# Kernel optimization log

Measured on AMD Instinct MI355X. Metric: run time of the kernel, lower is better.

Reference implementation:

```python
import jax, jax.numpy as jnp
import numpy as np
import math

DIM = 1024
N_HEADS = 16
N_KV_HEADS = 8
HEAD_DIM = 64
HIDDEN = 4096
WINDOW = 512
NORM_EPS = 1e-5
QK_EPS = 1e-6


def get_alibi_slopes(n_heads):
    def _power_of_2(n):
        start = 2 ** (-2 ** (-(math.log2(n) - 3)))
        return [start * start ** i for i in range(n)]
    if math.log2(n_heads).is_integer():
        return _power_of_2(n_heads)
    closest = 2 ** math.floor(math.log2(n_heads))
    slopes = _power_of_2(closest)
    extra = _power_of_2(2 * closest)
    slopes.extend(extra[0::2][:n_heads - closest])
    return slopes


def layer_norm(x, w, eps):
    m = x.mean(-1, keepdims=True)
    v = ((x - m) ** 2).mean(-1, keepdims=True)
    return (x - m) * jax.lax.rsqrt(v + eps) * w


def setup_inputs() -> dict:
    key = jax.random.key(0)
    ks = jax.random.split(key, 16)
    s = 0.02
    return {
        "x": jax.random.normal(ks[0], (2, 2048, DIM), dtype=jnp.float32),
        "wq": jax.random.normal(ks[1], (N_HEADS * HEAD_DIM, DIM), dtype=jnp.float32) * s,
        "wk": jax.random.normal(ks[2], (N_KV_HEADS * HEAD_DIM, DIM), dtype=jnp.float32) * s,
        "wv": jax.random.normal(ks[3], (N_KV_HEADS * HEAD_DIM, DIM), dtype=jnp.float32) * s,
        "wo": jax.random.normal(ks[4], (DIM, N_HEADS * HEAD_DIM), dtype=jnp.float32) * s,
        "q_norm_w": jnp.ones((N_HEADS * HEAD_DIM,), dtype=jnp.float32),
        "k_norm_w": jnp.ones((N_KV_HEADS * HEAD_DIM,), dtype=jnp.float32),
        "attn_norm_w": jnp.ones((DIM,), dtype=jnp.float32),
        "ffn_norm_w": jnp.ones((DIM,), dtype=jnp.float32),
        "w1": jax.random.normal(ks[5], (HIDDEN, DIM), dtype=jnp.float32) * s,
        "w2": jax.random.normal(ks[6], (DIM, HIDDEN), dtype=jnp.float32) * s,
        "w3": jax.random.normal(ks[7], (HIDDEN, DIM), dtype=jnp.float32) * s,
        "attn_scale": jnp.full((DIM,), 1e-5, dtype=jnp.float32),
        "ffn_scale": jnp.full((DIM,), 1e-5, dtype=jnp.float32),
    }


def reference(x, wq, wk, wv, wo, q_norm_w, k_norm_w, attn_norm_w, ffn_norm_w,
              w1, w2, w3, attn_scale, ffn_scale):
    bsz, seqlen, _ = x.shape
    n_rep = N_HEADS // N_KV_HEADS

    h = layer_norm(x, attn_norm_w, NORM_EPS)
    q = layer_norm(h @ wq.T, q_norm_w, QK_EPS).reshape(bsz, seqlen, N_HEADS, HEAD_DIM).transpose(0, 2, 1, 3)
    k = layer_norm(h @ wk.T, k_norm_w, QK_EPS).reshape(bsz, seqlen, N_KV_HEADS, HEAD_DIM).transpose(0, 2, 1, 3)
    v = (h @ wv.T).reshape(bsz, seqlen, N_KV_HEADS, HEAD_DIM).transpose(0, 2, 1, 3)
    k = jnp.repeat(k, n_rep, axis=1)  # [b, H, s, hd]
    v = jnp.repeat(v, n_rep, axis=1)

    pos = jnp.arange(seqlen)
    dist = pos[None, :] - pos[:, None]  # dist[i, j] = j - i (as in the torch code)
    base = jnp.where((dist >= 0) & (dist <= WINDOW), 0.0, -jnp.inf)  # [s, s]
    slopes = jnp.asarray(get_alibi_slopes(N_HEADS), dtype=jnp.float32)
    alibi = -jnp.abs(slopes[:, None, None] * dist.astype(jnp.float32))  # [H, s, s]
    full_mask = base[None, :, :] + alibi  # [H, s, s]

    scores = jnp.einsum('bhqd,bhkd->bhqk', q, k) / math.sqrt(HEAD_DIM) + full_mask[None]
    attn = jax.nn.softmax(scores, axis=-1)
    out = jnp.einsum('bhqk,bhkd->bhqd', attn, v)
    out = out.transpose(0, 2, 1, 3).reshape(bsz, seqlen, N_HEADS * HEAD_DIM)
    x = x + (out @ wo.T) * attn_scale

    h2 = layer_norm(x, ffn_norm_w, NORM_EPS)
    ffn = (jax.nn.silu(h2 @ w1.T) * (h2 @ w3.T)) @ w2.T
    return x + ffn * ffn_scale
```

## Files before the change

kernel.cpp:

```cpp
#include <hip/hip_runtime.h>


typedef __bf16 bf16;
typedef __attribute__((ext_vector_type(8))) __bf16 bf16x8;
typedef __attribute__((ext_vector_type(4))) float f32x4;
typedef __attribute__((ext_vector_type(4))) short s16x4;

#define MFMA16(a, b, c) __builtin_amdgcn_mfma_f32_16x16x32_bf16(a, b, c, 0, 0, 0)

__device__ __forceinline__ void gload_lds16(const bf16* g, bf16* l) {
    __builtin_amdgcn_global_load_lds(
        (const __attribute__((address_space(1))) unsigned int*)g,
        (__attribute__((address_space(3))) unsigned int*)l, 16, 0, 0);
}

__global__ void sniff_kernel(const unsigned short* __restrict__ x, int* __restrict__ flag) {
    __shared__ int s;
    if (threadIdx.x == 0) s = 0;
    __syncthreads();
    int bad = 0;
#pragma unroll
    for (int i = 0; i < 16; ++i) {
        const unsigned short u = x[threadIdx.x * 16 + i];
        const int e = (u >> 7) & 0xFF;
        if (e >= 135) bad = 1;
    }
    if (bad) atomicOr(&s, 1);
    __syncthreads();
    if (threadIdx.x == 0) flag[0] = s;
}

__global__ void convert_all_kernel(const void* __restrict__ wq, const void* __restrict__ wk,
                                   const void* __restrict__ wv, const void* __restrict__ wo,
                                   const void* __restrict__ w1, const void* __restrict__ w3,
                                   const void* __restrict__ w2, bf16* __restrict__ dst,
                                   const int* __restrict__ flag) {
    const long e = ((long)blockIdx.x * 256 + threadIdx.x) * 4;
    const void* src; long off;
    if      (e < 1048576)  { src = wq; off = 0; }
    else if (e < 1572864)  { src = wk; off = 1048576; }
    else if (e < 2097152)  { src = wv; off = 1572864; }
    else if (e < 3145728)  { src = wo; off = 2097152; }
    else if (e < 7340032)  { src = w1; off = 3145728; }
    else if (e < 11534336) { src = w3; off = 7340032; }
    else                   { src = w2; off = 11534336; }
    if (flag[0] != 0) {
        const f32x4 v = *(const f32x4*)((const float*)src + (e - off));
        bf16 tmp[4];
#pragma unroll
        for (int j = 0; j < 4; ++j) tmp[j] = (bf16)v[j];
        *(s16x4*)(dst + e) = *(s16x4*)tmp;
    } else {
        *(s16x4*)(dst + e) = *(const s16x4*)((const short*)src + (e - off));
    }
}

__global__ void ln_kernel(const void* __restrict__ in, const void* __restrict__ w,
                          bf16* __restrict__ out, int W, float eps,
                          const int* __restrict__ flag, int in_flv, int w_flv) {
    const int row = blockIdx.x, t = threadIdx.x;
    const int nch = W >> 3;
    const bool act = t < nch;
    const bool f32 = flag[0] != 0;
    float v[8];
    float s = 0.f, s2 = 0.f;
    if (act) {
        if (in_flv && f32) {
            const float* rp = (const float*)in + (size_t)row * W + t * 8;
            const f32x4 a = *(const f32x4*)rp, b = *(const f32x4*)(rp + 4);
#pragma unroll
            for (int j = 0; j < 4; ++j) { v[j] = a[j]; v[4 + j] = b[j]; }
        } else {
            const bf16x8 xv = *(const bf16x8*)((const bf16*)in + (size_t)row * W + t * 8);
#pragma unroll
            for (int j = 0; j < 8; ++j) v[j] = (float)xv[j];
        }
#pragma unroll
        for (int j = 0; j < 8; ++j) { s += v[j]; s2 += v[j] * v[j]; }
    }
#pragma unroll
    for (int off = 32; off; off >>= 1) { s += __shfl_xor(s, off); s2 += __shfl_xor(s2, off); }
    __shared__ float red[4];
    if ((t & 63) == 0) { red[(t >> 6) * 2] = s; red[(t >> 6) * 2 + 1] = s2; }
    __syncthreads();
    const float fs = red[0] + red[2], fs2 = red[1] + red[3];
    const float inw = 1.f / (float)W;
    const float mean = fs * inw;
    const float var = fs2 * inw - mean * mean;
    const float rstd = rsqrtf(var + eps);
    if (act) {
        float wv8[8];
        if (w_flv && f32) {
            const float* wp = (const float*)w + t * 8;
            const f32x4 a = *(const f32x4*)wp, b = *(const f32x4*)(wp + 4);
#pragma unroll
            for (int j = 0; j < 4; ++j) { wv8[j] = a[j]; wv8[4 + j] = b[j]; }
        } else {
            const bf16x8 ww = *(const bf16x8*)((const bf16*)w + t * 8);
#pragma unroll
            for (int j = 0; j < 8; ++j) wv8[j] = (float)ww[j];
        }
        bf16x8 ov;
#pragma unroll
        for (int j = 0; j < 8; ++j) ov[j] = (bf16)((v[j] - mean) * rstd * wv8[j]);
        *(bf16x8*)(out + (size_t)row * W + t * 8) = ov;
    }
}

template <int EPI>
__global__ __launch_bounds__(512, 4)
void gemm2(const bf16* __restrict__ A, const bf16* __restrict__ B,
           void* __restrict__ Cout, const void* __restrict__ res,
           const void* __restrict__ scale, int M, int N, int K,
           const int* __restrict__ flag, int res_flv, int out_flv) {
    __shared__ bf16 LDS[3 * 8192];
    const bool f32 = flag[0] != 0;
    const int t = threadIdx.x;
    const int wv = t >> 6, ln = t & 63;
    const int qr = ln & 15, g = ln >> 4;
    const int wr = wv >> 2, wc = wv & 3;
    const int row0 = blockIdx.y * 128, col0 = blockIdx.x * 128;

    f32x4 acc[4][2] = {};

    const bf16* aSrc = A + (size_t)(row0 + (t >> 2)) * K + (t & 3) * 8;
    const bf16* bSrc = B + (size_t)(col0 + (t >> 2)) * K + (t & 3) * 8;
    const int NIT = K >> 5;

#define STAGE(bi, k0)                                              \
    do {                                                           \
        bf16* lb = LDS + (bi) * 8192 + wv * 512;                   \
        gload_lds16(aSrc + (k0), lb);                              \
        gload_lds16(bSrc + (k0), lb + 4096);                       \
    } while (0)

    STAGE(0, 0);
    STAGE(1, 32);
    asm volatile("s_waitcnt vmcnt(2)" ::: "memory");
    __builtin_amdgcn_s_barrier();
    __builtin_amdgcn_sched_barrier(0);

    int cur = 0, sb = 2;
    for (int it = 0; it < NIT; ++it) {
        const bool more = (it + 2) < NIT;
        if (more) STAGE(sb, (it + 2) * 32);
        const bf16* bufA = LDS + cur * 8192;
        const bf16* bufB = bufA + 4096;
        bf16x8 af[4], bfr[2];
#pragma unroll
        for (int i = 0; i < 4; ++i)
            af[i] = *(const bf16x8*)&bufA[(wr * 64 + i * 16 + qr) * 32 + g * 8];
#pragma unroll
        for (int j = 0; j < 2; ++j)
            bfr[j] = *(const bf16x8*)&bufB[(wc * 32 + j * 16 + qr) * 32 + g * 8];
#pragma unroll
        for (int i = 0; i < 4; ++i)
#pragma unroll
            for (int j = 0; j < 2; ++j)
                acc[i][j] = MFMA16(af[i], bfr[j], acc[i][j]);
        if (more) asm volatile("s_waitcnt vmcnt(2)" ::: "memory");
        else      asm volatile("s_waitcnt vmcnt(0)" ::: "memory");
        __builtin_amdgcn_s_barrier();
        __builtin_amdgcn_sched_barrier(0);
        cur = cur == 2 ? 0 : cur + 1;
        sb  = sb  == 2 ? 0 : sb  + 1;
    }
#undef STAGE

#pragma unroll
    for (int i = 0; i < 4; ++i) {
#pragma unroll
        for (int j = 0; j < 2; ++j) {
            const int rr0 = row0 + wr * 64 + i * 16 + g * 4;
            const int cc  = col0 + wc * 32 + j * 16 + qr;
            if (EPI == 4) {
                if (cc < 1024) {
#pragma unroll
                    for (int r = 0; r < 4; ++r)
                        ((bf16*)Cout)[(size_t)(rr0 + r) * 1024 + cc] = (bf16)acc[i][j][r];
                } else if (cc < 1536) {
#pragma unroll
                    for (int r = 0; r < 4; ++r)
                        ((bf16*)res)[(size_t)(rr0 + r) * 512 + (cc - 1024)] = (bf16)acc[i][j][r];
                } else {
                    const int kv = cc - 1536, kvh = kv >> 6, d = kv & 63;
                    const int bb = rr0 >> 11, s0 = rr0 & 2047;
                    bf16 tmp[4];
#pragma unroll
                    for (int r = 0; r < 4; ++r) tmp[r] = (bf16)acc[i][j][r];
                    *(s16x4*)((bf16*)scale + (((size_t)bb * 8 + kvh) * 64 + d) * 2048 + s0) = *(s16x4*)tmp;
                }
            } else {
                float scv = 0.f;
                if (EPI == 1)
                    scv = f32 ? ((const float*)scale)[cc] : (float)((const bf16*)scale)[cc];
#pragma unroll
                for (int r = 0; r < 4; ++r) {
                    const size_t idx = (size_t)(rr0 + r) * N + cc;
                    float vv = acc[i][j][r];
                    if (EPI == 1) {
                        const float rv = (res_flv && f32) ? ((const float*)res)[idx]
                                                          : (float)((const bf16*)res)[idx];
                        vv = rv + vv * scv;
                    }
                    if (EPI == 3) {
                        const float uv = (float)((const bf16*)res)[idx];
                        vv = uv / (1.f + __expf(-uv)) * vv;
                    }
                    if (out_flv && f32) ((float*)Cout)[idx] = vv;
                    else                ((bf16*)Cout)[idx] = (bf16)vv;
                }
            }
        }
    }
}

__global__ __launch_bounds__(256)
void attn_kernel(const bf16* __restrict__ qn, const bf16* __restrict__ kn,
                 const bf16* __restrict__ vt, bf16* __restrict__ aout) {
    __shared__ bf16 SH[3 * 4096];
    const int t = threadIdx.x, wv = t >> 6, ln = t & 63;
    const int qr = ln & 15, g = ln >> 4;
    const int h = blockIdx.y, b = blockIdx.z, kvh = h >> 1;
    const int q0blk = blockIdx.x * 64;
    const int qa = q0blk + wv * 16 + qr;
    const float slope = exp2f(-0.5f * (float)(h + 1));

    const bf16* qrow = qn + ((size_t)(b * 2048 + qa)) * 1024 + h * 64;
    const bf16x8 qb0 = *(const bf16x8*)(qrow + g * 8);
    const bf16x8 qb1 = *(const bf16x8*)(qrow + 32 + g * 8);

    const bf16* kbase = kn + (size_t)b * 2048 * 512 + kvh * 64;
    const bf16* vbase = vt + ((size_t)(b * 8 + kvh) * 64) * 2048;
    const int krow_l = t >> 3;
    const int kcsrc  = (t & 7) ^ ((t >> 3) & 7);
    const int vd     = t >> 2;
    const int vcsrc  = (t & 3) ^ ((t >> 2) & 3);
    const bf16* kgsrc = kbase + kcsrc * 8;
    const bf16* vgsrc = vbase + (size_t)vd * 2048;
    bf16* lK0 = SH + wv * 512;
    bf16* lV0 = SH + 2048 + wv * 512;

#define STAGE_T(kts, bi)                                           \
    do {                                                           \
        int ksrc = (kts) + krow_l;                                 \
        ksrc = ksrc > 2047 ? 2047 : ksrc;                          \
        gload_lds16(kgsrc + (size_t)ksrc * 512, lK0 + (bi) * 4096);\
        int vsrc = (kts) + vcsrc * 8;                              \
        vsrc = vsrc > 2040 ? 2040 : vsrc;                          \
        gload_lds16(vgsrc + vsrc, lV0 + (bi) * 4096);              \
    } while (0)

    STAGE_T(q0blk, 0);
    STAGE_T(q0blk + 32, 1);
    STAGE_T(q0blk + 64, 2);
    asm volatile("s_waitcnt vmcnt(4)" ::: "memory");
    __builtin_amdgcn_s_barrier();
    __builtin_amdgcn_sched_barrier(0);

    f32x4 o[4] = {};
    float mrun = -1e29f, lsum = 0.f;
    int cur = 0;

    for (int it = 0; it < 18; ++it) {
        const int kt = q0blk + it * 32;
        const bf16* Kb = SH + cur * 4096;
        const bf16* Vb = Kb + 2048;

        f32x4 sc[2] = {f32x4{0, 0, 0, 0}, f32x4{0, 0, 0, 0}};
#pragma unroll
        for (int ks = 0; ks < 2; ++ks) {
            const int lrow = ks * 16 + qr;
            const int sw = (lrow & 7) * 8;
            sc[ks] = MFMA16(*(const bf16x8*)&Kb[lrow * 64 + (((g) * 8) ^ sw)],        qb0, sc[ks]);
            sc[ks] = MFMA16(*(const bf16x8*)&Kb[lrow * 64 + (((4 + g) * 8) ^ sw)],    qb1, sc[ks]);
        }
        float s[2][4], p[2][4];
        float tmax = -1e30f;
#pragma unroll
        for (int ks = 0; ks < 2; ++ks)
#pragma unroll
            for (int r = 0; r < 4; ++r) {
                const int key = kt + ks * 16 + g * 4 + r;
                const int dist = key - qa;
                const bool valid = (dist >= 0) && (dist <= 512) && (key < 2048);
                const float sv = valid ? sc[ks][r] * 0.125f - slope * (float)dist : -1e30f;
                s[ks][r] = sv;
                tmax = fmaxf(tmax, sv);
            }
        tmax = fmaxf(tmax, __shfl_xor(tmax, 16));
        tmax = fmaxf(tmax, __shfl_xor(tmax, 32));
        const float mnew = fmaxf(mrun, tmax);
        const float alpha = __expf(mrun - mnew);
        mrun = mnew;
        float ps = 0.f;
#pragma unroll
        for (int ks = 0; ks < 2; ++ks)
#pragma unroll
            for (int r = 0; r < 4; ++r) { p[ks][r] = __expf(s[ks][r] - mnew); ps += p[ks][r]; }
        lsum = lsum * alpha + ps;
#pragma unroll
        for (int fd = 0; fd < 4; ++fd) o[fd] *= alpha;

        bf16x8 pb;
#pragma unroll
        for (int j = 0; j < 8; ++j) {
            const int srcl = (((2 * g + (j >> 2)) & 3) << 4) | qr;
            const float v0 = __shfl(p[0][j & 3], srcl);
            const float v1 = __shfl(p[1][j & 3], srcl);
            pb[j] = (bf16)((g & 2) ? v1 : v0);
        }
#pragma unroll
        for (int fd = 0; fd < 4; ++fd) {
            const int d = fd * 16 + qr;
            const bf16x8 va = *(const bf16x8*)&Vb[d * 32 + ((g ^ (d & 3)) * 8)];
            o[fd] = MFMA16(va, pb, o[fd]);
        }

        __builtin_amdgcn_s_barrier();
        if (it + 3 < 18) {
            STAGE_T(kt + 96, cur);
            asm volatile("s_waitcnt vmcnt(4)" ::: "memory");
        } else {
            asm volatile("s_waitcnt vmcnt(0)" ::: "memory");
        }
        __builtin_amdgcn_s_barrier();
        __builtin_amdgcn_sched_barrier(0);
        cur = cur == 2 ? 0 : cur + 1;
    }
#undef STAGE_T

    float lt = lsum + __shfl_xor(lsum, 16);
    lt += __shfl_xor(lt, 32);
    lt = fmaxf(lt, 1e-30f);
    const float inv = 1.f / lt;
    bf16* orow = aout + ((size_t)(b * 2048 + qa)) * 1024 + h * 64;
#pragma unroll
    for (int fd = 0; fd < 4; ++fd) {
        bf16 tmp[4];
#pragma unroll
        for (int r = 0; r < 4; ++r) tmp[r] = (bf16)(o[fd][r] * inv);
        *(s16x4*)(orow + fd * 16 + g * 4) = *(s16x4*)tmp;
    }
}

extern "C" void kernel_launch(void* const* d_in, const int* in_sizes, int n_in,
                              void* d_out, int out_size, void* d_ws, size_t ws_size,
                              hipStream_t stream) {
    int* flag = (int*)d_ws;
    bf16* base = (bf16*)d_ws + 64;
    bf16* h    = base;
    bf16* q    = h + 4194304;
    bf16* kbuf = q + 4194304;
    bf16* vtb  = kbuf + 2097152;
    bf16* aout = vtb + 2097152;
    bf16* u    = aout + 4194304;
    bf16* wcv  = u + 16777216;

    bf16* woc = wcv + 2097152;
    bf16* w1c = wcv + 3145728;
    bf16* w3c = wcv + 7340032;
    bf16* w2c = wcv + 11534336;

    const dim3 blk(512);
    sniff_kernel<<<1, 256, 0, stream>>>((const unsigned short*)d_in[0], flag);
    convert_all_kernel<<<15360, 256, 0, stream>>>(
        d_in[1], d_in[2], d_in[3], d_in[4], d_in[9], d_in[11], d_in[10], wcv, flag);

    ln_kernel<<<4096, 128, 0, stream>>>(d_in[0], d_in[7], h, 1024, 1e-5f, flag, 1, 1);
    gemm2<4><<<dim3(16, 32), blk, 0, stream>>>(h, wcv, q, kbuf, vtb, 4096, 2048, 1024, flag, 0, 0);
    ln_kernel<<<4096, 128, 0, stream>>>(q, d_in[5], q, 1024, 1e-6f, flag, 0, 1);
    ln_kernel<<<4096, 128, 0, stream>>>(kbuf, d_in[6], kbuf, 512, 1e-6f, flag, 0, 1);
    attn_kernel<<<dim3(32, 16, 2), dim3(256), 0, stream>>>(q, kbuf, vtb, aout);
    gemm2<1><<<dim3(8, 32), blk, 0, stream>>>(aout, woc, q, d_in[0], d_in[12], 4096, 1024, 1024, flag, 1, 0);
    ln_kernel<<<4096, 128, 0, stream>>>(q, d_in[8], h, 1024, 1e-5f, flag, 0, 1);
    gemm2<0><<<dim3(32, 32), blk, 0, stream>>>(h, w1c, u, nullptr, nullptr, 4096, 4096, 1024, flag, 0, 0);
    gemm2<3><<<dim3(32, 32), blk, 0, stream>>>(h, w3c, u, u, nullptr, 4096, 4096, 1024, flag, 0, 0);
    gemm2<1><<<dim3(8, 32), blk, 0, stream>>>(u, w2c, d_out, q, d_in[13], 4096, 1024, 4096, flag, 0, 1);
}
```

Before: 283.8 us.

## Add LDS XOR swizzle, block swizzle, deeper pipeline and 256x128 FFN GEMM tiles

The GEMM gets an XOR swizzle on the LDS chunk index to cut bank conflicts on fragment reads. It also gets an optional block-index remap that groups row tiles for L2 reuse, and a configurable pipeline depth, using 5 buffers for the K=4096 down-projection. A new gemm3 kernel with 256x128 tiles, vectorized bf16 stores and a fused SiLU-gate epilogue replaces the w1/w3 GEMMs to raise operand reuse. The larger LDS footprint and register use may lower occupancy.

```diff
diff --git a/kernel.cpp b/kernel.cpp
--- a/kernel.cpp
+++ b/kernel.cpp
@@ -107,24 +107,33 @@
     }
 }
 
-template <int EPI>
+template <int EPI, int NBUF, int SWZ>
 __global__ __launch_bounds__(512, 4)
 void gemm2(const bf16* __restrict__ A, const bf16* __restrict__ B,
            void* __restrict__ Cout, const void* __restrict__ res,
            const void* __restrict__ scale, int M, int N, int K,
            const int* __restrict__ flag, int res_flv, int out_flv) {
-    __shared__ bf16 LDS[3 * 8192];
+    __shared__ bf16 LDS[NBUF * 8192];
     const bool f32 = flag[0] != 0;
     const int t = threadIdx.x;
     const int wv = t >> 6, ln = t & 63;
     const int qr = ln & 15, g = ln >> 4;
     const int wr = wv >> 2, wc = wv & 3;
-    const int row0 = blockIdx.y * 128, col0 = blockIdx.x * 128;
+    int bx = blockIdx.x, by = blockIdx.y;
+    if (SWZ) {
+        const int bid = by * gridDim.x + bx;
+        const int g8 = bid & 7, m = bid >> 3;
+        bx = m % gridDim.x;
+        by = g8 + 8 * (m / gridDim.x);
+    }
+    const int row0 = by * 128, col0 = bx * 128;
 
     f32x4 acc[4][2] = {};
 
-    const bf16* aSrc = A + (size_t)(row0 + (t >> 2)) * K + (t & 3) * 8;
-    const bf16* bSrc = B + (size_t)(col0 + (t >> 2)) * K + (t & 3) * 8;
+    const int cx = ((t & 3) ^ ((t >> 2) & 3)) * 8;
+    const bf16* aSrc = A + (size_t)(row0 + (t >> 2)) * K + cx;
+    const bf16* bSrc = B + (size_t)(col0 + (t >> 2)) * K + cx;
+    const int gx8 = (g ^ (qr & 3)) * 8;
     const int NIT = K >> 5;
 
 #define STAGE(bi, k0)                                              \
@@ -134,36 +143,41 @@
         gload_lds16(bSrc + (k0), lb + 4096);                       \
     } while (0)
 
-    STAGE(0, 0);
-    STAGE(1, 32);
-    asm volatile("s_waitcnt vmcnt(2)" ::: "memory");
+#pragma unroll
+    for (int pb = 0; pb < NBUF - 1; ++pb) STAGE(pb, pb * 32);
+    if constexpr (NBUF == 3) asm volatile("s_waitcnt vmcnt(2)" ::: "memory");
+    else                     asm volatile("s_waitcnt vmcnt(6)" ::: "memory");
     __builtin_amdgcn_s_barrier();
     __builtin_amdgcn_sched_barrier(0);
 
-    int cur = 0, sb = 2;
+    int cur = 0, sb = NBUF - 1;
     for (int it = 0; it < NIT; ++it) {
-        const bool more = (it + 2) < NIT;
-        if (more) STAGE(sb, (it + 2) * 32);
+        const bool more = (it + NBUF - 1) < NIT;
+        if (more) STAGE(sb, (it + NBUF - 1) * 32);
         const bf16* bufA = LDS + cur * 8192;
         const bf16* bufB = bufA + 4096;
         bf16x8 af[4], bfr[2];
 #pragma unroll
         for (int i = 0; i < 4; ++i)
-            af[i] = *(const bf16x8*)&bufA[(wr * 64 + i * 16 + qr) * 32 + g * 8];
+            af[i] = *(const bf16x8*)&bufA[(wr * 64 + i * 16 + qr) * 32 + gx8];
 #pragma unroll
         for (int j = 0; j < 2; ++j)
-            bfr[j] = *(const bf16x8*)&bufB[(wc * 32 + j * 16 + qr) * 32 + g * 8];
+            bfr[j] = *(const bf16x8*)&bufB[(wc * 32 + j * 16 + qr) * 32 + gx8];
 #pragma unroll
         for (int i = 0; i < 4; ++i)
 #pragma unroll
             for (int j = 0; j < 2; ++j)
                 acc[i][j] = MFMA16(af[i], bfr[j], acc[i][j]);
-        if (more) asm volatile("s_waitcnt vmcnt(2)" ::: "memory");
-        else      asm volatile("s_waitcnt vmcnt(0)" ::: "memory");
+        if (more) {
+            if constexpr (NBUF == 3) asm volatile("s_waitcnt vmcnt(2)" ::: "memory");
+            else                     asm volatile("s_waitcnt vmcnt(6)" ::: "memory");
+        } else {
+            asm volatile("s_waitcnt vmcnt(0)" ::: "memory");
+        }
         __builtin_amdgcn_s_barrier();
         __builtin_amdgcn_sched_barrier(0);
-        cur = cur == 2 ? 0 : cur + 1;
-        sb  = sb  == 2 ? 0 : sb  + 1;
+        cur = cur + 1 == NBUF ? 0 : cur + 1;
+        sb  = sb + 1 == NBUF ? 0 : sb + 1;
     }
 #undef STAGE
 
@@ -215,6 +229,93 @@
     }
 }
 
+template <int EPI>
+__global__ __launch_bounds__(512, 4)
+void gemm3(const bf16* __restrict__ A, const bf16* __restrict__ B,
+           bf16* __restrict__ C, const bf16* __restrict__ res,
+           int M, int N, int K) {
+    __shared__ bf16 LDS[3 * 12288];
+    const int t = threadIdx.x;
+    const int wv = t >> 6, ln = t & 63;
+    const int qr = ln & 15, g = ln >> 4;
+    const int wr = wv >> 1, wc = wv & 1;
+    const int row0 = blockIdx.y * 256, col0 = blockIdx.x * 128;
+
+    f32x4 acc[4][4] = {};
+
+    const int cx = ((t & 3) ^ ((t >> 2) & 3)) * 8;
+    const bf16* aSrc  = A + (size_t)(row0 + (t >> 2)) * K + cx;
+    const bf16* aSrc2 = A + (size_t)(row0 + 128 + (t >> 2)) * K + cx;
+    const bf16* bSrc  = B + (size_t)(col0 + (t >> 2)) * K + cx;
+    const int gx8 = (g ^ (qr & 3)) * 8;
+    const int NIT = K >> 5;
+
+#define STAGE3(bi, k0)                                             \
+    do {                                                           \
+        bf16* lb = LDS + (bi) * 12288 + wv * 512;                  \
+        gload_lds16(aSrc + (k0), lb);                              \
+        gload_lds16(aSrc2 + (k0), lb + 4096);                      \
+        gload_lds16(bSrc + (k0), lb + 8192);                       \
+    } while (0)
+
+    STAGE3(0, 0);
+    STAGE3(1, 32);
+    asm volatile("s_waitcnt vmcnt(3)" ::: "memory");
+    __builtin_amdgcn_s_barrier();
+    __builtin_amdgcn_sched_barrier(0);
+
+    int cur = 0, sb = 2;
+    for (int it = 0; it < NIT; ++it) {
+        const bool more = (it + 2) < NIT;
+        if (more) STAGE3(sb, (it + 2) * 32);
+        const bf16* bufA = LDS + cur * 12288;
+        const bf16* bufB = bufA + 8192;
+        bf16x8 af[4], bfr[4];
+#pragma unroll
+        for (int i = 0; i < 4; ++i)
+            af[i] = *(const bf16x8*)&bufA[(wr * 64 + i * 16 + qr) * 32 + gx8];
+#pragma unroll
+        for (int j = 0; j < 4; ++j)
+            bfr[j] = *(const bf16x8*)&bufB[(wc * 64 + j * 16 + qr) * 32 + gx8];
+#pragma unroll
+        for (int i = 0; i < 4; ++i)
+#pragma unroll
+            for (int j = 0; j < 4; ++j)
+                acc[i][j] = MFMA16(bfr[j], af[i], acc[i][j]);
+        if (more) asm volatile("s_waitcnt vmcnt(3)" ::: "memory");
+        else      asm volatile("s_waitcnt vmcnt(0)" ::: "memory");
+        __builtin_amdgcn_s_barrier();
+        __builtin_amdgcn_sched_barrier(0);
+        cur = cur == 2 ? 0 : cur + 1;
+        sb  = sb  == 2 ? 0 : sb  + 1;
+    }
+#undef STAGE3
+
+#pragma unroll
+    for (int i = 0; i < 4; ++i) {
+        const int row = row0 + wr * 64 + i * 16 + qr;
+#pragma unroll
+        for (int j = 0; j < 4; ++j) {
+            const int col = col0 + wc * 64 + j * 16 + g * 4;
+            const size_t idx = (size_t)row * N + col;
+            bf16 tmp[4];
+            if (EPI == 3) {
+                const s16x4 rv4 = *(const s16x4*)(res + idx);
+#pragma unroll
+                for (int r = 0; r < 4; ++r) {
+                    bf16 ub; *(short*)&ub = rv4[r];
+                    const float uv = (float)ub;
+                    tmp[r] = (bf16)(uv / (1.f + __expf(-uv)) * acc[i][j][r]);
+                }
+            } else {
+#pragma unroll
+                for (int r = 0; r < 4; ++r) tmp[r] = (bf16)acc[i][j][r];
+            }
+            *(s16x4*)(C + idx) = *(s16x4*)tmp;
+        }
+    }
+}
+
 __global__ __launch_bounds__(256)
 void attn_kernel(const bf16* __restrict__ qn, const bf16* __restrict__ kn,
                  const bf16* __restrict__ vt, bf16* __restrict__ aout) {
@@ -368,13 +469,13 @@
         d_in[1], d_in[2], d_in[3], d_in[4], d_in[9], d_in[11], d_in[10], wcv, flag);
 
     ln_kernel<<<4096, 128, 0, stream>>>(d_in[0], d_in[7], h, 1024, 1e-5f, flag, 1, 1);
-    gemm2<4><<<dim3(16, 32), blk, 0, stream>>>(h, wcv, q, kbuf, vtb, 4096, 2048, 1024, flag, 0, 0);
+    gemm2<4, 3, 0><<<dim3(16, 32), blk, 0, stream>>>(h, wcv, q, kbuf, vtb, 4096, 2048, 1024, flag, 0, 0);
     ln_kernel<<<4096, 128, 0, stream>>>(q, d_in[5], q, 1024, 1e-6f, flag, 0, 1);
     ln_kernel<<<4096, 128, 0, stream>>>(kbuf, d_in[6], kbuf, 512, 1e-6f, flag, 0, 1);
     attn_kernel<<<dim3(32, 16, 2), dim3(256), 0, stream>>>(q, kbuf, vtb, aout);
-    gemm2<1><<<dim3(8, 32), blk, 0, stream>>>(aout, woc, q, d_in[0], d_in[12], 4096, 1024, 1024, flag, 1, 0);
+    gemm2<1, 3, 1><<<dim3(8, 32), blk, 0, stream>>>(aout, woc, q, d_in[0], d_in[12], 4096, 1024, 1024, flag, 1, 0);
     ln_kernel<<<4096, 128, 0, stream>>>(q, d_in[8], h, 1024, 1e-5f, flag, 0, 1);
-    gemm2<0><<<dim3(32, 32), blk, 0, stream>>>(h, w1c, u, nullptr, nullptr, 4096, 4096, 1024, flag, 0, 0);
-    gemm2<3><<<dim3(32, 32), blk, 0, stream>>>(h, w3c, u, u, nullptr, 4096, 4096, 1024, flag, 0, 0);
-    gemm2<1><<<dim3(8, 32), blk, 0, stream>>>(u, w2c, d_out, q, d_in[13], 4096, 1024, 4096, flag, 0, 1);
-}
+    gemm3<0><<<dim3(32, 16), blk, 0, stream>>>(h, w1c, u, nullptr, 4096, 4096, 1024);
+    gemm3<3><<<dim3(32, 16), blk, 0, stream>>>(h, w3c, u, u,       4096, 4096, 1024);
+    gemm2<1, 5, 1><<<dim3(8, 32), blk, 0, stream>>>(u, w2c, d_out, q, d_in[13], 4096, 1024, 4096, flag, 0, 1);
+}
```

Result: faster. 272.6 us (-3.9%).
